# Optimization experiments

Measured on AMD Instinct MI355X. Metric: run time of the kernel, lower is better.

## Reference

```python
import jax, jax.numpy as jnp
import numpy as np

N, D, K = 4096, 1024, 32
MARGIN = 0.3
OP_TYPE = "weighty"


def setup_inputs() -> dict:
    key = jax.random.key(0)
    k1, k2, k3, k4, k5 = jax.random.split(key, 5)
    return {
        "inputs": jax.random.normal(k1, (N, D), jnp.float32),
        "prediction": jax.random.normal(k2, (N, K), jnp.float32),
        "targets": jax.random.randint(k3, (N,), 0, K),
        "true_targets": jax.random.randint(k4, (N,), 0, K),
        "prob": jax.random.uniform(k5, (N,), jnp.float32),
        "threshold": jnp.float32(0.5),
    }


def _weighty(d1, d2, pair_type, op_type):
    # vectorized translation of weighty_new
    if op_type == "mean":
        return (d1 + d2) / 2.0
    if op_type == "max":
        return jnp.maximum(d1, d2)
    if op_type == "min":
        return jnp.minimum(d1, d2)
    if op_type == "max-min":
        return jnp.maximum(d1, d2) if pair_type == 1 else jnp.minimum(d1, d2)
    # op_type == 'weighty'
    if pair_type == 1:
        e1, e2 = jnp.exp(d1), jnp.exp(d2)
        return (e1 * d1 + e2 * d2) / (e1 + e2)
    e1, e2 = jnp.exp(-d1), jnp.exp(-d2)
    return (e1 * d1 + e2 * d2) / (e1 + e2 + 1e-6)


def reference(inputs, prediction, targets, true_targets, prob, threshold):
    n = inputs.shape[0]
    rows = jnp.arange(n)
    # pairwise euclidean dist (GEMM-based, matches addmm_ formulation)
    sq = jnp.sum(inputs * inputs, axis=1)
    dist = sq[:, None] + sq[None, :] - 2.0 * (inputs @ inputs.T)
    dist = jnp.sqrt(jnp.clip(dist, 1e-12, None))  # [n, n]

    same = targets[:, None] == targets[None, :]
    conf = prob >= threshold

    # negatives sorted ascending by dist; positives sorted descending by dist
    neg_order = jnp.argsort(jnp.where(~same, dist, jnp.inf), axis=1)   # [n,n]
    pos_order = jnp.argsort(jnp.where(same, -dist, jnp.inf), axis=1)   # [n,n]
    hp = pos_order[:, 0]   # hardest positive (max dist)
    hn = neg_order[:, 0]   # hardest negative (min dist)
    d_ap = dist[rows, hp]
    d_an = dist[rows, hn]

    cp = prob[hp] >= threshold
    cn = prob[hn] >= threshold
    fn = jnp.argmax(prediction, axis=1)[hn] == targets  # hard neg is a false negative

    # neg re-selection: ranks 1..10 first with prob>=t, else rank 11 (loop_cnt cap 10)
    neg_cand = neg_order[:, 1:12]                       # [n,11]
    ok_n = prob[neg_cand] >= threshold
    sel_n = jnp.where(ok_n[:, :10].any(axis=1), jnp.argmax(ok_n[:, :10], axis=1), 10)
    d_nn = dist[rows, neg_cand[rows, sel_n]]

    # pos re-selection: descending ranks 1..5 first with prob>=t, else rank 6 (loop_cnt cap 5)
    pos_cand = pos_order[:, 1:7]                        # [n,6]
    ok_p = prob[pos_cand] >= threshold
    sel_p = jnp.where(ok_p[:, :5].any(axis=1), jnp.argmax(ok_p[:, :5], axis=1), 5)
    d_np = dist[rows, pos_cand[rows, sel_p]]

    w1 = _weighty(d_ap, d_an, 1, OP_TYPE)
    w0 = _weighty(d_ap, d_an, 0, OP_TYPE)

    case_b = cp & (~cn) & fn                 # confident pos, unconfident FN neg
    case_cd = (~cp) & (cn | (~fn))           # unconfident pos branches that re-select pos
    inv = (~cp) & (~cn) & fn                 # inverse loss branch

    ap = jnp.where(case_b, w1, jnp.where(case_cd, d_np, d_ap))
    an = jnp.where(case_b, d_nn, jnp.where(case_cd, w0, d_an))

    per = jnp.where(inv,
                    jax.nn.relu(an - ap + MARGIN),
                    jax.nn.relu(ap - an + MARGIN))
    conff = conf.astype(per.dtype)
    cnt = jnp.sum(conf.astype(jnp.int32))
    loss = jnp.where(cnt > 0, jnp.sum(per * conff) / jnp.maximum(cnt, 1).astype(per.dtype), 0.0)
    correct = jnp.sum(((an >= ap) & conf).astype(jnp.int32))
    return loss, correct, cnt
```

## Files before the change

kernel.cpp:

```cpp
#include <hip/hip_runtime.h>
#include <hip/hip_bf16.h>
#include <stdint.h>

typedef _Float16 half8 __attribute__((ext_vector_type(8)));
typedef _Float16 half4 __attribute__((ext_vector_type(4)));
typedef float f32x4 __attribute__((ext_vector_type(4)));
typedef unsigned short ushort8v __attribute__((ext_vector_type(8)));
typedef unsigned short ushort4v __attribute__((ext_vector_type(4)));
typedef unsigned long long u64;

#define N_ROWS 4096
#define DIM 1024
#define KCLS 32
#define MARGIN_F 0.3f

typedef const __attribute__((address_space(1))) void GASV;
typedef __attribute__((address_space(3))) void LASV;

__device__ __forceinline__ void gload_lds16(const void* g, void* l) {
    __builtin_amdgcn_global_load_lds((GASV*)g, (LASV*)l, 16, 0, 0);
}

__global__ __launch_bounds__(256) void prep_kernel(
    const float* __restrict__ inputs, const float* __restrict__ prediction,
    _Float16* __restrict__ xh, float* __restrict__ sq, int* __restrict__ pred_cls)
{
    int wid = threadIdx.x >> 6, lane = threadIdx.x & 63;
    int r = blockIdx.x * 4 + wid;
    const float* row = inputs + (size_t)r * DIM;
    _Float16* hrow = xh + (size_t)r * DIM;
    float s = 0.f;
#pragma unroll
    for (int c = 0; c < 4; ++c) {
        int idx = lane * 4 + c * 256;
        float4 v = *(const float4*)(row + idx);
        s += v.x * v.x + v.y * v.y + v.z * v.z + v.w * v.w;
        half4 h;
        h.x = (_Float16)v.x; h.y = (_Float16)v.y;
        h.z = (_Float16)v.z; h.w = (_Float16)v.w;
        *(half4*)(hrow + idx) = h;
    }
#pragma unroll
    for (int off = 32; off; off >>= 1) s += __shfl_xor(s, off);

    u64 key = 0ull;
    if (lane < KCLS) {
        unsigned b = __float_as_uint(prediction[(size_t)r * KCLS + lane]);
        unsigned u = (b & 0x80000000u) ? ~b : (b | 0x80000000u);
        key = ((u64)u << 32) | (unsigned)(KCLS - 1 - lane);
    }
#pragma unroll
    for (int off = 32; off; off >>= 1) {
        u64 o = __shfl_xor(key, off);
        if (o > key) key = o;
    }
    if (lane == 0) {
        sq[r] = s;
        pred_cls[r] = KCLS - 1 - (int)(key & 0xFFFFFFFFu);
    }
}

__global__ __launch_bounds__(512) void gemm_kernel(
    const _Float16* __restrict__ X, const float* __restrict__ sq,
    const int* __restrict__ targets,
    unsigned short* __restrict__ out, int mode, int rb0)
{
    __shared__ __align__(16) _Float16 As[4 * 128 * 32];
    __shared__ __align__(16) _Float16 Bs[4 * 128 * 32];
    int tid = threadIdx.x;

    int bx, by;
    bool mirror = false;
    if (mode == 0) {
        int u = ((int)blockIdx.x & 7) * 66 + ((int)blockIdx.x >> 3);
        int t_ = (int)((sqrtf(8.f * u + 1.f) - 1.f) * 0.5f);
        while ((t_ + 1) * (t_ + 2) / 2 <= u) ++t_;
        while (t_ * (t_ + 1) / 2 > u) --t_;
        by = t_;
        bx = u - t_ * (t_ + 1) / 2;
        mirror = (bx != by);
    } else {
        int nwg = gridDim.x;
        int q = nwg >> 3;
        int swz = ((int)blockIdx.x & 7) * q + ((int)blockIdx.x >> 3);
        int nbx = nwg / 32;
        bx = swz % nbx;
        by = swz / nbx;
    }

    int rs = tid >> 2;
    int ss = tid & 3;
    int srcslot = ss ^ (rs & 3);
    const _Float16* gA = X + (size_t)(rb0 + bx * 128 + rs) * DIM + srcslot * 8;
    const _Float16* gB = X + (size_t)(by * 128 + rs) * DIM + srcslot * 8;
    _Float16* lA = As + tid * 8;
    _Float16* lB = Bs + tid * 8;

    int wid = tid >> 6, lane = tid & 63;
    int wr = (wid >> 2) * 64, wc = (wid & 3) * 32;
    int fr = lane & 15, q4 = lane >> 4;

    f32x4 acc[4][2];
#pragma unroll
    for (int m = 0; m < 4; ++m)
#pragma unroll
        for (int n = 0; n < 2; ++n) acc[m][n] = (f32x4){0.f, 0.f, 0.f, 0.f};

    auto STAGE = [&](int buf, int t) {
        int k0 = t * 32;
        gload_lds16(gA + k0, lA + buf * 4096);
        gload_lds16(gB + k0, lB + buf * 4096);
    };
    auto COMPUTE = [&](int buf) {
        const _Float16* Ac = As + buf * 4096;
        const _Float16* Bc = Bs + buf * 4096;
        half8 a[4], b[2];
#pragma unroll
        for (int m = 0; m < 4; ++m) {
            int row = wr + m * 16 + fr;
            int s = q4 ^ (row & 3);
            a[m] = *(const half8*)(Ac + row * 32 + s * 8);
        }
#pragma unroll
        for (int n = 0; n < 2; ++n) {
            int brow = wc + n * 16 + fr;
            int s = q4 ^ (brow & 3);
            b[n] = *(const half8*)(Bc + brow * 32 + s * 8);
        }
        __builtin_amdgcn_s_setprio(1);
#pragma unroll
        for (int m = 0; m < 4; ++m)
#pragma unroll
            for (int n = 0; n < 2; ++n)
                acc[m][n] = __builtin_amdgcn_mfma_f32_16x16x32_f16(a[m], b[n], acc[m][n], 0, 0, 0);
        __builtin_amdgcn_s_setprio(0);
    };

    STAGE(0, 0); STAGE(1, 1); STAGE(2, 2); STAGE(3, 3);

    for (int t = 0; t < 28; ++t) {
        asm volatile("s_waitcnt vmcnt(6)" ::: "memory");
        __builtin_amdgcn_s_barrier();
        __builtin_amdgcn_sched_barrier(0);
        COMPUTE(t & 3);
        __builtin_amdgcn_sched_barrier(0);
        __builtin_amdgcn_s_barrier();
        __builtin_amdgcn_sched_barrier(0);
        STAGE(t & 3, t + 4);
    }
    asm volatile("s_waitcnt vmcnt(6)" ::: "memory");
    __builtin_amdgcn_s_barrier();
    __builtin_amdgcn_sched_barrier(0);
    COMPUTE(0);
    __builtin_amdgcn_s_barrier();
    asm volatile("s_waitcnt vmcnt(4)" ::: "memory");
    __builtin_amdgcn_s_barrier();
    __builtin_amdgcn_sched_barrier(0);
    COMPUTE(1);
    __builtin_amdgcn_s_barrier();
    asm volatile("s_waitcnt vmcnt(2)" ::: "memory");
    __builtin_amdgcn_s_barrier();
    __builtin_amdgcn_sched_barrier(0);
    COMPUTE(2);
    __builtin_amdgcn_s_barrier();
    asm volatile("s_waitcnt vmcnt(0)" ::: "memory");
    __builtin_amdgcn_s_barrier();
    __builtin_amdgcn_sched_barrier(0);
    COMPUTE(3);

    int rbase = rb0 + bx * 128 + wr + q4 * 4;
    float sqr_[4][4];
    int trr[4][4];
#pragma unroll
    for (int m = 0; m < 4; ++m)
#pragma unroll
        for (int q = 0; q < 4; ++q) {
            sqr_[m][q] = sq[rbase + m * 16 + q];
            trr[m][q] = targets[rbase + m * 16 + q];
        }

#pragma unroll
    for (int n = 0; n < 2; ++n) {
        int col = by * 128 + wc + n * 16 + fr;
        float sqc = sq[col];
        int tc = targets[col];
#pragma unroll
        for (int m = 0; m < 4; ++m) {
            int row0 = rbase + m * 16;
            ushort4v hv;
#pragma unroll
            for (int q = 0; q < 4; ++q) {
                float d2v = fmaxf(sqr_[m][q] + sqc - 2.f * acc[m][n][q], 1e-12f);
                _Float16 h = (_Float16)d2v;
                unsigned short hb = __builtin_bit_cast(unsigned short, h);
                hb = (unsigned short)(hb | ((trr[m][q] == tc) ? 0x8000u : 0u));
                hv[q] = hb;
                out[(size_t)(row0 + q) * N_ROWS + col] = hb;
            }
            if (mirror)
                *(ushort4v*)&out[(size_t)col * N_ROWS + row0] = hv;
        }
    }
}

__global__ __launch_bounds__(256) void select_kernel(
    const unsigned short* __restrict__ dot,
    const int* __restrict__ targets, const float* __restrict__ prob,
    const int* __restrict__ pred_cls, const float* __restrict__ thr_p,
    int rb0, float* __restrict__ per_term, int* __restrict__ corr_flag)
{
    __shared__ unsigned Tn[4], Tp[4];
    __shared__ unsigned negCand[64];
    __shared__ unsigned posCand[64];
    __shared__ unsigned cnts[2];
    __shared__ unsigned sN[12], sP[7];
    __shared__ unsigned red[4];
    __shared__ unsigned bcast;

    int t = threadIdx.x, lane = t & 63, w = t >> 6;
    int rloc = blockIdx.x, r = rb0 + rloc;
    const unsigned short* drow = dot + (size_t)rloc * N_ROWS;

    if (t < 64) { negCand[t] = 0xFFFFFFFFu; posCand[t] = 0u; }
    if (t < 2) cnts[t] = 0u;

    unsigned short hb[16];
    unsigned mneg = 0xFFFFFFFFu, mpos = 0u;
    {
        ushort8v v0 = *(const ushort8v*)(drow + t * 8);
        ushort8v v1 = *(const ushort8v*)(drow + 2048 + t * 8);
#pragma unroll
        for (int j = 0; j < 8; ++j) {
            unsigned b = v0[j]; hb[j] = (unsigned short)b;
            mneg = b < mneg ? b : mneg;
            mpos = b > mpos ? b : mpos;
        }
#pragma unroll
        for (int j = 0; j < 8; ++j) {
            unsigned b = v1[j]; hb[8 + j] = (unsigned short)b;
            mneg = b < mneg ? b : mneg;
            mpos = b > mpos ? b : mpos;
        }
    }

    unsigned T3 = 0xFFFFFFFFu, m = mneg;
#pragma unroll
    for (int rd = 0; rd < 3; ++rd) {
        unsigned b = m;
#pragma unroll
        for (int off = 32; off; off >>= 1) {
            unsigned o = __shfl_xor(b, off);
            b = o < b ? o : b;
        }
        T3 = b;
        if (m == b) m = 0xFFFFFFFFu;
    }
    unsigned P2 = 0u, mp = mpos;
#pragma unroll
    for (int rd = 0; rd < 2; ++rd) {
        unsigned b = mp;
#pragma unroll
        for (int off = 32; off; off >>= 1) {
            unsigned o = __shfl_xor(b, off);
            b = o > b ? o : b;
        }
        P2 = b;
        if (mp == b) mp = 0u;
    }
    if (lane == 0) { Tn[w] = T3; Tp[w] = P2; }
    __syncthreads();

    unsigned TnB = Tn[0];
    TnB = Tn[1] > TnB ? Tn[1] : TnB;
    TnB = Tn[2] > TnB ? Tn[2] : TnB;
    TnB = Tn[3] > TnB ? Tn[3] : TnB;
    unsigned TpB = Tp[0];
    TpB = Tp[1] < TpB ? Tp[1] : TpB;
    TpB = Tp[2] < TpB ? Tp[2] : TpB;
    TpB = Tp[3] < TpB ? Tp[3] : TpB;

#pragma unroll
    for (int j = 0; j < 16; ++j) {
        int col = (j < 8) ? (t * 8 + j) : (2048 + t * 8 + (j - 8));
        unsigned b = hb[j];
        if (!(b & 0x8000u) && b <= TnB) {
            unsigned s = atomicAdd(&cnts[0], 1u);
            if (s < 64u) negCand[s] = (b << 16) | (unsigned)col;
        }
        if ((b & 0x8000u) && b >= TpB) {
            unsigned s = atomicAdd(&cnts[1], 1u);
            if (s < 64u) posCand[s] = (b << 16) | (unsigned)(N_ROWS - 1 - col);
        }
    }
    __syncthreads();

    bool fb = (cnts[0] > 64u) || (cnts[1] > 64u);

    if (!fb) {
        if (w == 0) {
            unsigned v = negCand[lane];
#pragma unroll
            for (int k = 2; k <= 64; k <<= 1) {
#pragma unroll
                for (int j = 32; j; j >>= 1) {
                    if (j >= k) continue;
                    unsigned o = __shfl_xor(v, j);
                    bool up = (lane & k) == 0;
                    bool small = (lane & j) == 0;
                    bool keepmin = (small == up);
                    unsigned lo = v < o ? v : o, hi = v < o ? o : v;
                    v = keepmin ? lo : hi;
                }
            }
            if (lane < 12) sN[lane] = v;
        } else if (w == 1) {
            unsigned v = ~posCand[lane];
#pragma unroll
            for (int k = 2; k <= 64; k <<= 1) {
#pragma unroll
                for (int j = 32; j; j >>= 1) {
                    if (j >= k) continue;
                    unsigned o = __shfl_xor(v, j);
                    bool up = (lane & k) == 0;
                    bool small = (lane & j) == 0;
                    bool keepmin = (small == up);
                    unsigned lo = v < o ? v : o, hi = v < o ? o : v;
                    v = keepmin ? lo : hi;
                }
            }
            if (lane < 7) sP[lane] = ~v;
        }
    } else {
        unsigned remN = 0, remP = 0;
        for (int rd = 0; rd < 12; ++rd) {
            unsigned best = 0xFFFFFFFFu;
#pragma unroll
            for (int j = 0; j < 16; ++j) {
                int col = (j < 8) ? (t * 8 + j) : (2048 + t * 8 + (j - 8));
                unsigned b = hb[j];
                bool valid = !(b & 0x8000u) && !((remN >> j) & 1u);
                unsigned nk = valid ? ((b << 16) | (unsigned)col) : 0xFFFFFFFFu;
                best = nk < best ? nk : best;
            }
#pragma unroll
            for (int off = 32; off; off >>= 1) {
                unsigned o = __shfl_xor(best, off);
                best = o < best ? o : best;
            }
            if (lane == 0) red[w] = best;
            __syncthreads();
            if (t == 0) {
                unsigned b0 = red[0];
                b0 = red[1] < b0 ? red[1] : b0;
                b0 = red[2] < b0 ? red[2] : b0;
                b0 = red[3] < b0 ? red[3] : b0;
                sN[rd] = b0; bcast = b0;
            }
            __syncthreads();
            unsigned b0 = bcast;
#pragma unroll
            for (int j = 0; j < 16; ++j) {
                int col = (j < 8) ? (t * 8 + j) : (2048 + t * 8 + (j - 8));
                if ((((unsigned)hb[j] << 16) | (unsigned)col) == b0) remN |= 1u << j;
            }
            __syncthreads();
        }
        for (int rd = 0; rd < 7; ++rd) {
            unsigned best = 0u;
#pragma unroll
            for (int j = 0; j < 16; ++j) {
                int col = (j < 8) ? (t * 8 + j) : (2048 + t * 8 + (j - 8));
                unsigned b = hb[j];
                bool valid = (b & 0x8000u) && !((remP >> j) & 1u);
                unsigned pk = valid ? ((b << 16) | (unsigned)(N_ROWS - 1 - col)) : 0u;
                best = pk > best ? pk : best;
            }
#pragma unroll
            for (int off = 32; off; off >>= 1) {
                unsigned o = __shfl_xor(best, off);
                best = o > best ? o : best;
            }
            if (lane == 0) red[w] = best;
            __syncthreads();
            if (t == 0) {
                unsigned b0 = red[0];
                b0 = red[1] > b0 ? red[1] : b0;
                b0 = red[2] > b0 ? red[2] : b0;
                b0 = red[3] > b0 ? red[3] : b0;
                sP[rd] = b0; bcast = b0;
            }
            __syncthreads();
            unsigned b0 = bcast;
#pragma unroll
            for (int j = 0; j < 16; ++j) {
                int col = (j < 8) ? (t * 8 + j) : (2048 + t * 8 + (j - 8));
                if ((((unsigned)hb[j] << 16) | (unsigned)(N_ROWS - 1 - col)) == b0) remP |= 1u << j;
            }
            __syncthreads();
        }
    }
    __syncthreads();

    if (w == 0) {
        float thr = *thr_p;
        int tr = targets[r];
        unsigned kN = (lane < 12) ? sN[lane] : 0xFFFFFFFFu;
        unsigned kP = (lane >= 32 && lane < 39) ? sP[lane - 32] : 0u;
        int idxN = (int)(kN & 0xFFFFu) & (N_ROWS - 1);
        int idxP = (N_ROWS - 1 - (int)(kP & 0xFFFFu)) & (N_ROWS - 1);
        bool confN = (lane < 12) && kN != 0xFFFFFFFFu && (prob[idxN] >= thr);
        bool confP = (lane >= 32 && lane < 39) && kP != 0u && (prob[idxP] >= thr);
        u64 balN = __ballot(confN);
        u64 balP = __ballot(confP);

        u64 mN_ = balN & 0x7FEull;
        int selN = mN_ ? (__ffsll(mN_) - 1) : 11;
        unsigned dnn_b = __shfl(kN >> 16, selN);
        u64 mP_ = balP & (0x3Eull << 32);
        int selP = mP_ ? (__ffsll(mP_) - 1) : 38;
        unsigned dnp_b = __shfl(kP >> 16, selP);
        unsigned dap_b = __shfl(kP >> 16, 32);

        if (lane == 0) {
            auto h2f = [](unsigned b16) -> float {
                unsigned short us = (unsigned short)(b16 & 0x7FFFu);
                _Float16 h = __builtin_bit_cast(_Float16, us);
                return (float)h;
            };
            float d_ap = sqrtf(h2f(dap_b));
            float d_an = sqrtf(h2f(kN >> 16));
            int hn = idxN;
            bool cp = (balP >> 32) & 1ull;
            bool cn = balN & 1ull;
            bool fn = (pred_cls[hn] == tr);
            float d_nn = sqrtf(h2f(dnn_b));
            float d_np = sqrtf(h2f(dnp_b));

            float e1p = __expf(d_ap), e2p = __expf(d_an);
            float w1 = (e1p * d_ap + e2p * d_an) / (e1p + e2p);
            float e1n = __expf(-d_ap), e2n = __expf(-d_an);
            float w0 = (e1n * d_ap + e2n * d_an) / (e1n + e2n + 1e-6f);
            bool case_b = cp && !cn && fn;
            bool case_cd = !cp && (cn || !fn);
            bool inv = !cp && !cn && fn;
            float ap = case_b ? w1 : (case_cd ? d_np : d_ap);
            float an = case_b ? d_nn : (case_cd ? w0 : d_an);
            float per = inv ? fmaxf(an - ap + MARGIN_F, 0.f)
                            : fmaxf(ap - an + MARGIN_F, 0.f);
            per_term[r] = per;
            corr_flag[r] = (an >= ap) ? 1 : 0;
        }
    }
}

__global__ __launch_bounds__(256) void finalize_kernel(
    const float* __restrict__ per_term, const int* __restrict__ corr_flag,
    const float* __restrict__ prob, const float* __restrict__ thr_p,
    float* __restrict__ out)
{
    __shared__ float sred[4]; __shared__ int cred[4]; __shared__ int nred[4];
    float thr = *thr_p;
    int t = threadIdx.x, lane = t & 63, wid = t >> 6;
    float s = 0.f; int c = 0, n = 0;
    for (int i = t; i < N_ROWS; i += 256) {
        if (prob[i] >= thr) {
            s += per_term[i];
            c += corr_flag[i];
            n += 1;
        }
    }
#pragma unroll
    for (int off = 32; off; off >>= 1) {
        s += __shfl_xor(s, off);
        c += __shfl_xor(c, off);
        n += __shfl_xor(n, off);
    }
    if (lane == 0) { sred[wid] = s; cred[wid] = c; nred[wid] = n; }
    __syncthreads();
    if (t == 0) {
        float ss = sred[0] + sred[1] + sred[2] + sred[3];
        int cc = cred[0] + cred[1] + cred[2] + cred[3];
        int nn = nred[0] + nred[1] + nred[2] + nred[3];
        float loss = (nn > 0) ? ss / (float)nn : 0.f;
        out[0] = loss;
        out[1] = (float)cc;
        out[2] = (float)nn;
    }
}

extern "C" void kernel_launch(void* const* d_in, const int* in_sizes, int n_in,
                              void* d_out, int out_size, void* d_ws, size_t ws_size,
                              hipStream_t stream)
{
    const float* inputs     = (const float*)d_in[0];
    const float* prediction = (const float*)d_in[1];
    const int*   targets    = (const int*)d_in[2];
    const float* prob       = (const float*)d_in[4];
    const float* thr        = (const float*)d_in[5];
    float* out = (float*)d_out;

    char* ws = (char*)d_ws;
    size_t off = 0;
    auto alloc = [&](size_t bytes) -> char* {
        char* p = ws + off;
        off = (off + bytes + 255) & ~(size_t)255;
        return p;
    };
    _Float16* xh     = (_Float16*)alloc((size_t)N_ROWS * DIM * sizeof(_Float16));
    float* sq        = (float*)alloc((size_t)N_ROWS * 4);
    int*   pred_cls  = (int*)alloc((size_t)N_ROWS * 4);
    float* per_term  = (float*)alloc((size_t)N_ROWS * 4);
    int*   corr_flag = (int*)alloc((size_t)N_ROWS * 4);

    size_t avail = (ws_size > off) ? (ws_size - off) : 0;
    size_t rowbytes = (size_t)N_ROWS * 2;
    int RB = 128;
    while (RB * 2 <= N_ROWS && (size_t)(RB * 2) * rowbytes <= avail) RB *= 2;
    unsigned short* dotbuf = (unsigned short*)alloc((size_t)RB * rowbytes);

    hipLaunchKernelGGL(prep_kernel, dim3(N_ROWS / 4), dim3(256), 0, stream,
                       inputs, prediction, xh, sq, pred_cls);
    if (RB == N_ROWS) {
        hipLaunchKernelGGL(gemm_kernel, dim3(528), dim3(512), 0, stream,
                           xh, sq, targets, dotbuf, 0, 0);
        hipLaunchKernelGGL(select_kernel, dim3(N_ROWS), dim3(256), 0, stream,
                           dotbuf, targets, prob, pred_cls, thr, 0,
                           per_term, corr_flag);
    } else {
        for (int rb0 = 0; rb0 < N_ROWS; rb0 += RB) {
            hipLaunchKernelGGL(gemm_kernel, dim3((RB / 128) * 32), dim3(512), 0, stream,
                               xh, sq, targets, dotbuf, 1, rb0);
            hipLaunchKernelGGL(select_kernel, dim3(RB), dim3(256), 0, stream,
                               dotbuf, targets, prob, pred_cls, thr, rb0,
                               per_term, corr_flag);
        }
    }
    hipLaunchKernelGGL(finalize_kernel, dim3(1), dim3(256), 0, stream,
                       per_term, corr_flag, prob, thr, out);
}
```

Baseline: 77.28 us.

## Switch GEMM to three-stage LDS ring with one barrier per k-step

The distance GEMM's LDS staging moves from a four-buffer pipeline with two barriers per iteration to a three-buffer rotating ring with a single barrier per k-step. Each new global-to-LDS load is issued right after compute into the buffer consumed one step earlier. The LDS swizzle changes to XOR on (row>>1)&3 instead of row&3, and the MFMA priority bumps are dropped. In the selection kernel, each distance value now updates only the negative-min or the positive-max, chosen by its high bit, instead of both. This trades prefetch depth and LDS footprint for less synchronization, with some risk of exposed load latency.

```diff
diff --git a/kernel.cpp b/kernel.cpp
--- a/kernel.cpp
+++ b/kernel.cpp
@@ -65,8 +65,8 @@
     const int* __restrict__ targets,
     unsigned short* __restrict__ out, int mode, int rb0)
 {
-    __shared__ __align__(16) _Float16 As[4 * 128 * 32];
-    __shared__ __align__(16) _Float16 Bs[4 * 128 * 32];
+    __shared__ __align__(16) _Float16 As[3 * 128 * 32];
+    __shared__ __align__(16) _Float16 Bs[3 * 128 * 32];
     int tid = threadIdx.x;
 
     int bx, by;
@@ -90,7 +90,7 @@
 
     int rs = tid >> 2;
     int ss = tid & 3;
-    int srcslot = ss ^ (rs & 3);
+    int srcslot = ss ^ ((rs >> 1) & 3);
     const _Float16* gA = X + (size_t)(rb0 + bx * 128 + rs) * DIM + srcslot * 8;
     const _Float16* gB = X + (size_t)(by * 128 + rs) * DIM + srcslot * 8;
     _Float16* lA = As + tid * 8;
@@ -106,8 +106,8 @@
 #pragma unroll
         for (int n = 0; n < 2; ++n) acc[m][n] = (f32x4){0.f, 0.f, 0.f, 0.f};
 
-    auto STAGE = [&](int buf, int t) {
-        int k0 = t * 32;
+    auto STAGE = [&](int buf, int step) {
+        int k0 = step * 32;
         gload_lds16(gA + k0, lA + buf * 4096);
         gload_lds16(gB + k0, lB + buf * 4096);
     };
@@ -118,55 +118,40 @@
 #pragma unroll
         for (int m = 0; m < 4; ++m) {
             int row = wr + m * 16 + fr;
-            int s = q4 ^ (row & 3);
+            int s = q4 ^ ((row >> 1) & 3);
             a[m] = *(const half8*)(Ac + row * 32 + s * 8);
         }
 #pragma unroll
         for (int n = 0; n < 2; ++n) {
             int brow = wc + n * 16 + fr;
-            int s = q4 ^ (brow & 3);
+            int s = q4 ^ ((brow >> 1) & 3);
             b[n] = *(const half8*)(Bc + brow * 32 + s * 8);
         }
-        __builtin_amdgcn_s_setprio(1);
 #pragma unroll
         for (int m = 0; m < 4; ++m)
 #pragma unroll
             for (int n = 0; n < 2; ++n)
                 acc[m][n] = __builtin_amdgcn_mfma_f32_16x16x32_f16(a[m], b[n], acc[m][n], 0, 0, 0);
-        __builtin_amdgcn_s_setprio(0);
     };
 
-    STAGE(0, 0); STAGE(1, 1); STAGE(2, 2); STAGE(3, 3);
-
-    for (int t = 0; t < 28; ++t) {
-        asm volatile("s_waitcnt vmcnt(6)" ::: "memory");
+    STAGE(0, 0);
+    STAGE(1, 1);
+
+    int cc = 0, cs = 2;
+    for (int t = 0; t < 31; ++t) {
+        asm volatile("s_waitcnt vmcnt(2)" ::: "memory");
         __builtin_amdgcn_s_barrier();
         __builtin_amdgcn_sched_barrier(0);
-        COMPUTE(t & 3);
+        COMPUTE(cc);
         __builtin_amdgcn_sched_barrier(0);
-        __builtin_amdgcn_s_barrier();
-        __builtin_amdgcn_sched_barrier(0);
-        STAGE(t & 3, t + 4);
-    }
-    asm volatile("s_waitcnt vmcnt(6)" ::: "memory");
-    __builtin_amdgcn_s_barrier();
-    __builtin_amdgcn_sched_barrier(0);
-    COMPUTE(0);
-    __builtin_amdgcn_s_barrier();
-    asm volatile("s_waitcnt vmcnt(4)" ::: "memory");
-    __builtin_amdgcn_s_barrier();
-    __builtin_amdgcn_sched_barrier(0);
-    COMPUTE(1);
-    __builtin_amdgcn_s_barrier();
-    asm volatile("s_waitcnt vmcnt(2)" ::: "memory");
-    __builtin_amdgcn_s_barrier();
-    __builtin_amdgcn_sched_barrier(0);
-    COMPUTE(2);
-    __builtin_amdgcn_s_barrier();
+        if (t + 2 < 32) STAGE(cs, t + 2);
+        cc = (cc == 2) ? 0 : cc + 1;
+        cs = (cs == 2) ? 0 : cs + 1;
+    }
     asm volatile("s_waitcnt vmcnt(0)" ::: "memory");
     __builtin_amdgcn_s_barrier();
     __builtin_amdgcn_sched_barrier(0);
-    COMPUTE(3);
+    COMPUTE(cc);
 
     int rbase = rb0 + bx * 128 + wr + q4 * 4;
     float sqr_[4][4];
@@ -232,14 +217,12 @@
 #pragma unroll
         for (int j = 0; j < 8; ++j) {
             unsigned b = v0[j]; hb[j] = (unsigned short)b;
-            mneg = b < mneg ? b : mneg;
-            mpos = b > mpos ? b : mpos;
+            if (b & 0x8000u) mpos = mpos > b ? mpos : b; else mneg = mneg < b ? mneg : b;
         }
 #pragma unroll
         for (int j = 0; j < 8; ++j) {
             unsigned b = v1[j]; hb[8 + j] = (unsigned short)b;
-            mneg = b < mneg ? b : mneg;
-            mpos = b > mpos ? b : mpos;
+            if (b & 0x8000u) mpos = mpos > b ? mpos : b; else mneg = mneg < b ? mneg : b;
         }
     }
 
```

Result: no change. 76.53 us (-1.0%).
